# Kernel tuning notes

Measured on AMD Instinct MI355X. Metric: run time of the kernel, lower is better.

## Reference

```python
import jax, jax.numpy as jnp
import numpy as np

N_QUBITS = 8
DEPTH = 3
FEATURE_DIM = 512
NUM_CLASSES = 10
BATCH = 8192
CDTYPE = jnp.complex64


def _ry_batched(theta):
    # theta: (B,) -> (B,2,2) real RY matrices cast to complex
    c = jnp.cos(theta / 2)
    s = jnp.sin(theta / 2)
    row0 = jnp.stack([c, -s], axis=-1)
    row1 = jnp.stack([s, c], axis=-1)
    return jnp.stack([row0, row1], axis=-2).astype(CDTYPE)


def _ry(theta):
    c = jnp.cos(theta / 2).astype(CDTYPE)
    s = jnp.sin(theta / 2).astype(CDTYPE)
    return jnp.stack([jnp.stack([c, -s]), jnp.stack([s, c])])


def _rx(theta):
    c = jnp.cos(theta / 2).astype(CDTYPE)
    js = (-1j) * jnp.sin(theta / 2).astype(CDTYPE)
    return jnp.stack([jnp.stack([c, js]), jnp.stack([js, c])])


def _apply_1q(state, U, q, n):
    # state: (B, 2,...,2) little-endian: axis (n - q) holds qubit q's bit
    ax = n - q
    sm = jnp.moveaxis(state, ax, -1)
    if U.ndim == 3:  # per-batch gate
        new = jnp.einsum('b...k,bjk->b...j', sm, U)
    else:  # shared gate
        new = jnp.einsum('...k,jk->...j', sm, U)
    return jnp.moveaxis(new, -1, ax)


def _cnot(state, c, t, n):
    ax_c = n - c
    ax_t = n - t
    s0, s1 = jnp.split(state, 2, axis=ax_c)
    s1 = jnp.flip(s1, axis=ax_t)  # X on target where control=1
    return jnp.concatenate([s0, s1], axis=ax_c)


def _quantum_expect(angles, qnn_w, n=N_QUBITS, depth=DEPTH):
    # angles: (B, n) encoding angles; qnn_w: (depth*n*3,) circuit weights
    B = angles.shape[0]
    state = jnp.zeros((B,) + (2,) * n, CDTYPE)
    state = state.at[(slice(None),) + (0,) * n].set(1.0)
    # RY encoding layer (batched angles)
    for q in range(n):
        state = _apply_1q(state, _ry_batched(angles[:, q]), q, n)
    wr = qnn_w.reshape(depth, n, 3)
    for l in range(depth):
        for q in range(n):
            state = _apply_1q(state, _rx(wr[l, q, 0]), q, n)
            state = _apply_1q(state, _ry(wr[l, q, 1]), q, n)
            state = _apply_1q(state, _rx(wr[l, q, 2]), q, n)
        for q in range(n - 1):
            state = _cnot(state, q, q + 1, n)
        state = _cnot(state, n - 1, 0, n)
    # PauliZ expectation per qubit: sum probs weighted by (+1, -1) on that qubit's axis
    p = state.real ** 2 + state.imag ** 2  # (B, 2,...,2) real
    z = jnp.array([1.0, -1.0], p.dtype)
    outs = []
    for q in range(n):
        ax = n - q
        sign = z.reshape((1,) * ax + (2,) + (1,) * q)
        outs.append(jnp.sum(p * sign, axis=tuple(range(1, n + 1))))
    return jnp.stack(outs, axis=-1)  # (B, n)


def setup_inputs() -> dict:
    key = jax.random.key(0)
    k1, k2, k3, k4, k5 = jax.random.split(key, 5)
    x = jax.random.normal(k1, (BATCH, FEATURE_DIM), jnp.float32)
    bound_p = 1.0 / np.sqrt(FEATURE_DIM)
    proj_w = jax.random.uniform(k2, (N_QUBITS, FEATURE_DIM), jnp.float32, -bound_p, bound_p)
    qnn_w = 0.01 * jax.random.normal(k3, (DEPTH * N_QUBITS * 3,), jnp.float32)
    bound_o = 1.0 / np.sqrt(N_QUBITS)
    out_w = jax.random.uniform(k4, (NUM_CLASSES, N_QUBITS), jnp.float32, -bound_o, bound_o)
    out_b = jax.random.uniform(k5, (NUM_CLASSES,), jnp.float32, -bound_o, bound_o)
    return {'x': x, 'proj_w': proj_w, 'qnn_w': qnn_w, 'out_w': out_w, 'out_b': out_b}


def reference(x, proj_w, qnn_w, out_w, out_b):
    angles = jnp.tanh(x @ proj_w.T) * (jnp.pi / 2)  # (B, n_qubits)
    q_out = _quantum_expect(angles, qnn_w)          # (B, n_qubits)
    return q_out @ out_w.T + out_b                  # (B, num_classes)
```

## Files before the change

### kernel.cpp

```cpp
#include <hip/hip_runtime.h>
#include <math.h>

#define NQ 8
#define NDEPTH 3
#define FEAT 512
#define NCLS 10
#define NBATCH 8192


template <int CTRL, int ROW_MASK>
__device__ __forceinline__ float dpp_term(float v) {
    return __int_as_float(__builtin_amdgcn_update_dpp(
        0, __float_as_int(v), CTRL, ROW_MASK, 0xf, true));
}

__device__ __forceinline__ float wave_sum_bcast(float v) {
    v += dpp_term<0x111, 0xf>(v);
    v += dpp_term<0x112, 0xf>(v);
    v += dpp_term<0x114, 0xf>(v);
    v += dpp_term<0x118, 0xf>(v);
    v += dpp_term<0x142, 0xa>(v);
    v += dpp_term<0x143, 0xc>(v);
    return __int_as_float(__builtin_amdgcn_readlane(__float_as_int(v), 63));
}

__device__ __forceinline__ float bcastlane(float v, int srclane) {
    return __int_as_float(__builtin_amdgcn_readlane(__float_as_int(v), srclane));
}

template <int CTRL>
__device__ __forceinline__ float dpp_xor(float v) {
    return __int_as_float(__builtin_amdgcn_update_dpp(
        0, __float_as_int(v), CTRL, 0xf, 0xf, true));
}

__device__ __forceinline__ float fast_tanh(float v) {
    float e = __expf(2.f * v);
    return 1.f - 2.f / (e + 1.f);
}

__device__ __forceinline__ void cgate_pair(const float* __restrict__ u,
        float& r0, float& i0, float& r1, float& i1) {
    float nr0 = u[0]*r0 - u[1]*i0 + u[2]*r1 - u[3]*i1;
    float ni0 = u[0]*i0 + u[1]*r0 + u[2]*i1 + u[3]*r1;
    float nr1 = u[4]*r0 - u[5]*i0 + u[6]*r1 - u[7]*i1;
    float ni1 = u[4]*i0 + u[5]*r0 + u[6]*i1 + u[7]*r1;
    r0 = nr0; i0 = ni0; r1 = nr1; i1 = ni1;
}

__device__ __forceinline__ void cgate_shfl(const float* __restrict__ u, int bit,
        int mask, float (&re)[4], float (&im)[4]) {
    float dr  = bit ? u[6] : u[0], di = bit ? u[7] : u[1];
    float orr = bit ? u[4] : u[2], oi = bit ? u[5] : u[3];
#pragma unroll
    for (int j = 0; j < 4; j++) {
        float pr = __shfl_xor(re[j], mask);
        float pi = __shfl_xor(im[j], mask);
        float nr = dr*re[j] - di*im[j] + orr*pr - oi*pi;
        float ni = dr*im[j] + di*re[j] + orr*pi + oi*pr;
        re[j] = nr; im[j] = ni;
    }
}

template <int CTRL>
__device__ __forceinline__ void cgate_dpp(const float* __restrict__ u, int bit,
        float (&re)[4], float (&im)[4]) {
    float dr  = bit ? u[6] : u[0], di = bit ? u[7] : u[1];
    float orr = bit ? u[4] : u[2], oi = bit ? u[5] : u[3];
#pragma unroll
    for (int j = 0; j < 4; j++) {
        float pr = dpp_xor<CTRL>(re[j]);
        float pi = dpp_xor<CTRL>(im[j]);
        float nr = dr*re[j] - di*im[j] + orr*pr - oi*pi;
        float ni = dr*im[j] + di*re[j] + orr*pi + oi*pr;
        re[j] = nr; im[j] = ni;
    }
}

__global__ __launch_bounds__(256) void qsim_kernel(
        const float* __restrict__ x, const float* __restrict__ proj_w,
        const float* __restrict__ qnn_w, const float* __restrict__ out_w,
        const float* __restrict__ out_b, float* __restrict__ out) {
    __shared__ float gl[NDEPTH * NQ * 8];

    int tid = threadIdx.x;
    if (tid < NDEPTH * NQ) {
        float t0 = 0.5f * qnn_w[tid * 3 + 0];
        float t1 = 0.5f * qnn_w[tid * 3 + 1];
        float t2 = 0.5f * qnn_w[tid * 3 + 2];
        float c0 = cosf(t0), s0 = sinf(t0);
        float c1 = cosf(t1), s1 = sinf(t1);
        float c2 = cosf(t2), s2 = sinf(t2);
        float m00r =  c1 * c0, m00i =  s1 * s0;
        float m01r = -s1 * c0, m01i = -c1 * s0;
        float m10r =  s1 * c0, m10i = -c1 * s0;
        float m11r =  c1 * c0, m11i = -s1 * s0;
        float* g = gl + tid * 8;
        g[0] =  c2 * m00r + s2 * m10i;  g[1] =  c2 * m00i - s2 * m10r;
        g[2] =  c2 * m01r + s2 * m11i;  g[3] =  c2 * m01i - s2 * m11r;
        g[4] =  s2 * m00i + c2 * m10r;  g[5] = -s2 * m00r + c2 * m10i;
        g[6] =  s2 * m01i + c2 * m11r;  g[7] = -s2 * m01r + c2 * m11i;
    }
    __syncthreads();

    int lane = tid & 63;
    int b = blockIdx.x * 4 + (tid >> 6);

    const float4* xr4 = (const float4*)(x + (size_t)b * FEAT);
    float4 xa = xr4[lane], xb = xr4[lane + 64];
    float dq[8];
#pragma unroll
    for (int q = 0; q < 8; q++) {
        const float4* pw4 = (const float4*)(proj_w + q * FEAT);
        float4 wa = pw4[lane], wb = pw4[lane + 64];
        float acc = xa.x*wa.x + xa.y*wa.y + xa.z*wa.z + xa.w*wa.w
                  + xb.x*wb.x + xb.y*wb.y + xb.z*wb.z + xb.w*wb.w;
        dq[q] = wave_sum_bcast(acc);
    }
    int qsel = lane >> 3;
    float a0 = (qsel & 4) ? dq[4] : dq[0];
    float a1 = (qsel & 4) ? dq[5] : dq[1];
    float a2 = (qsel & 4) ? dq[6] : dq[2];
    float a3 = (qsel & 4) ? dq[7] : dq[3];
    float b0 = (qsel & 2) ? a2 : a0;
    float b1 = (qsel & 2) ? a3 : a1;
    float dsel = (qsel & 1) ? b1 : b0;
    float th = fast_tanh(dsel) * 0.78539816339744830962f;
    float se = __sinf(th), ce = __cosf(th);
    float cq[8], sq[8];
#pragma unroll
    for (int q = 0; q < 8; q++) {
        cq[q] = bcastlane(ce, q * 8);
        sq[q] = bcastlane(se, q * 8);
    }

    float F = 1.f;
#pragma unroll
    for (int q = 2; q < 8; q++) {
        int bit = (lane >> (q - 2)) & 1;
        F *= bit ? sq[q] : cq[q];
    }
    float re[4], im[4];
    re[0] = F * cq[0] * cq[1];
    re[1] = F * sq[0] * cq[1];
    re[2] = F * cq[0] * sq[1];
    re[3] = F * sq[0] * sq[1];
    im[0] = im[1] = im[2] = im[3] = 0.f;

#pragma unroll
    for (int l = 0; l < NDEPTH; l++) {
        const float* g = gl + l * NQ * 8;
        cgate_pair(g, re[0], im[0], re[1], im[1]);
        cgate_pair(g, re[2], im[2], re[3], im[3]);
        cgate_pair(g + 8,  re[0], im[0], re[2], im[2]);
        cgate_pair(g + 8,  re[1], im[1], re[3], im[3]);
        cgate_dpp<0xB1>(g + 16, lane & 1,        re, im);
        cgate_dpp<0x4E>(g + 24, (lane >> 1) & 1, re, im);
        cgate_shfl(g + 32, (lane >> 2) & 1, 4,  re, im);
        cgate_shfl(g + 40, (lane >> 3) & 1, 8,  re, im);
        cgate_shfl(g + 48, (lane >> 4) & 1, 16, re, im);
        cgate_shfl(g + 56, (lane >> 5) & 1, 32, re, im);
        { float t = re[1]; re[1] = re[3]; re[3] = t;
          t = im[1]; im[1] = im[3]; im[3] = t; }
        int base  = lane ^ ((lane << 1) & 63);
        int base2 = base ^ 1;
        re[0] = __shfl(re[0], base);  im[0] = __shfl(im[0], base);
        re[1] = __shfl(re[1], base);  im[1] = __shfl(im[1], base);
        re[2] = __shfl(re[2], base2); im[2] = __shfl(im[2], base2);
        re[3] = __shfl(re[3], base2); im[3] = __shfl(im[3], base2);
        int bit5 = (lane >> 5) & 1;
        {
            float t0 = bit5 ? re[1] : re[0], t1 = bit5 ? re[0] : re[1];
            float t2 = bit5 ? re[3] : re[2], t3 = bit5 ? re[2] : re[3];
            re[0] = t0; re[1] = t1; re[2] = t2; re[3] = t3;
            t0 = bit5 ? im[1] : im[0]; t1 = bit5 ? im[0] : im[1];
            t2 = bit5 ? im[3] : im[2]; t3 = bit5 ? im[2] : im[3];
            im[0] = t0; im[1] = t1; im[2] = t2; im[3] = t3;
        }
    }

    float p0 = re[0]*re[0] + im[0]*im[0];
    float p1 = re[1]*re[1] + im[1]*im[1];
    float p2 = re[2]*re[2] + im[2]*im[2];
    float p3 = re[3]*re[3] + im[3]*im[3];
    float pt = p0 + p1 + p2 + p3;
    float eq[8];
    eq[0] = wave_sum_bcast(p0 - p1 + p2 - p3);
    eq[1] = wave_sum_bcast(p0 + p1 - p2 - p3);
#pragma unroll
    for (int q = 2; q < 8; q++) {
        int bit = (lane >> (q - 2)) & 1;
        eq[q] = wave_sum_bcast(bit ? -pt : pt);
    }

    if (lane < NCLS) {
        const float* wrow = out_w + lane * NQ;
        float acc = out_b[lane];
#pragma unroll
        for (int q = 0; q < 8; q++) acc = fmaf(eq[q], wrow[q], acc);
        out[(size_t)b * NCLS + lane] = acc;
    }
}

extern "C" void kernel_launch(void* const* d_in, const int* in_sizes, int n_in,
                              void* d_out, int out_size, void* d_ws, size_t ws_size,
                              hipStream_t stream) {
    const float* x      = (const float*)d_in[0];
    const float* proj_w = (const float*)d_in[1];
    const float* qnn_w  = (const float*)d_in[2];
    const float* out_w  = (const float*)d_in[3];
    const float* out_b  = (const float*)d_in[4];
    float* out = (float*)d_out;

    qsim_kernel<<<NBATCH / 4, 256, 0, stream>>>(x, proj_w, qnn_w, out_w, out_b, out);
}
```

Baseline: 83.88 us.

## Process two samples per wave with swizzle-based gates and segmented reductions

Each wavefront now simulates two batch samples, interleaving their gate updates so cross-lane latency is hidden and proj_w loads are shared. Eight separate wave reductions for the projection are replaced by a segmented transpose-reduce, and the readout uses a butterfly with sign multipliers instead of six full reductions. Shuffles with masks 4/8/16 become ds_swizzle ops, gate matrices are loaded as float4 from LDS, and cos/sin use fast intrinsics. The cost is higher register pressure and half the grid size, with fewer waves available to hide latency.

```diff
diff --git a/kernel.cpp b/kernel.cpp
--- a/kernel.cpp
+++ b/kernel.cpp
@@ -34,12 +34,24 @@
         0, __float_as_int(v), CTRL, 0xf, 0xf, true));
 }
 
+template <int PAT>
+__device__ __forceinline__ float swz(float v) {
+    return __int_as_float(__builtin_amdgcn_ds_swizzle(__float_as_int(v), PAT));
+}
+
 __device__ __forceinline__ float fast_tanh(float v) {
     float e = __expf(2.f * v);
     return 1.f - 2.f / (e + 1.f);
 }
 
-__device__ __forceinline__ void cgate_pair(const float* __restrict__ u,
+__device__ __forceinline__ void load_u(const float* g, float (&u)[8]) {
+    float4 a = *(const float4*)g;
+    float4 b = *(const float4*)(g + 4);
+    u[0] = a.x; u[1] = a.y; u[2] = a.z; u[3] = a.w;
+    u[4] = b.x; u[5] = b.y; u[6] = b.z; u[7] = b.w;
+}
+
+__device__ __forceinline__ void cgate_pair(const float (&u)[8],
         float& r0, float& i0, float& r1, float& i1) {
     float nr0 = u[0]*r0 - u[1]*i0 + u[2]*r1 - u[3]*i1;
     float ni0 = u[0]*i0 + u[1]*r0 + u[2]*i1 + u[3]*r1;
@@ -48,22 +60,37 @@
     r0 = nr0; i0 = ni0; r1 = nr1; i1 = ni1;
 }
 
-__device__ __forceinline__ void cgate_shfl(const float* __restrict__ u, int bit,
-        int mask, float (&re)[4], float (&im)[4]) {
+template <int PAT>
+__device__ __forceinline__ void cgate_swz(const float (&u)[8], int bit,
+        float (&re)[4], float (&im)[4]) {
     float dr  = bit ? u[6] : u[0], di = bit ? u[7] : u[1];
     float orr = bit ? u[4] : u[2], oi = bit ? u[5] : u[3];
 #pragma unroll
     for (int j = 0; j < 4; j++) {
-        float pr = __shfl_xor(re[j], mask);
-        float pi = __shfl_xor(im[j], mask);
+        float pr = swz<PAT>(re[j]);
+        float pi = swz<PAT>(im[j]);
         float nr = dr*re[j] - di*im[j] + orr*pr - oi*pi;
         float ni = dr*im[j] + di*re[j] + orr*pi + oi*pr;
         re[j] = nr; im[j] = ni;
     }
 }
 
+__device__ __forceinline__ void cgate_shfl32(const float (&u)[8], int bit,
+        float (&re)[4], float (&im)[4]) {
+    float dr  = bit ? u[6] : u[0], di = bit ? u[7] : u[1];
+    float orr = bit ? u[4] : u[2], oi = bit ? u[5] : u[3];
+#pragma unroll
+    for (int j = 0; j < 4; j++) {
+        float pr = __shfl_xor(re[j], 32);
+        float pi = __shfl_xor(im[j], 32);
+        float nr = dr*re[j] - di*im[j] + orr*pr - oi*pi;
+        float ni = dr*im[j] + di*re[j] + orr*pi + oi*pr;
+        re[j] = nr; im[j] = ni;
+    }
+}
+
 template <int CTRL>
-__device__ __forceinline__ void cgate_dpp(const float* __restrict__ u, int bit,
+__device__ __forceinline__ void cgate_dpp(const float (&u)[8], int bit,
         float (&re)[4], float (&im)[4]) {
     float dr  = bit ? u[6] : u[0], di = bit ? u[7] : u[1];
     float orr = bit ? u[4] : u[2], oi = bit ? u[5] : u[3];
@@ -77,7 +104,77 @@
     }
 }
 
-__global__ __launch_bounds__(256) void qsim_kernel(
+__device__ __forceinline__ float seg_reduce8(const float (&a)[8], int lane) {
+    bool h5 = (lane & 32) != 0, h4 = (lane & 16) != 0, h3 = (lane & 8) != 0;
+    float r4[4];
+#pragma unroll
+    for (int k = 0; k < 4; k++) {
+        float snd = h5 ? a[k] : a[4 + k];
+        float rcv = __shfl_xor(snd, 32);
+        float kp  = h5 ? a[4 + k] : a[k];
+        r4[k] = kp + rcv;
+    }
+    float r2[2];
+#pragma unroll
+    for (int k = 0; k < 2; k++) {
+        float snd = h4 ? r4[k] : r4[2 + k];
+        float rcv = swz<0x401F>(snd);
+        float kp  = h4 ? r4[2 + k] : r4[k];
+        r2[k] = kp + rcv;
+    }
+    float snd = h3 ? r2[0] : r2[1];
+    float rcv = swz<0x201F>(snd);
+    float kp  = h3 ? r2[1] : r2[0];
+    float r = kp + rcv;
+    r += swz<0x101F>(r);
+    r += dpp_xor<0x4E>(r);
+    r += dpp_xor<0xB1>(r);
+    return r;
+}
+
+__device__ __forceinline__ void cnot_ladder(int lane, int base, int base2,
+        float (&re)[4], float (&im)[4]) {
+    float t = re[1]; re[1] = re[3]; re[3] = t;
+    t = im[1]; im[1] = im[3]; im[3] = t;
+    re[0] = __shfl(re[0], base);  im[0] = __shfl(im[0], base);
+    re[1] = __shfl(re[1], base);  im[1] = __shfl(im[1], base);
+    re[2] = __shfl(re[2], base2); im[2] = __shfl(im[2], base2);
+    re[3] = __shfl(re[3], base2); im[3] = __shfl(im[3], base2);
+    int bit5 = (lane >> 5) & 1;
+    float t0 = bit5 ? re[1] : re[0], t1 = bit5 ? re[0] : re[1];
+    float t2 = bit5 ? re[3] : re[2], t3 = bit5 ? re[2] : re[3];
+    re[0] = t0; re[1] = t1; re[2] = t2; re[3] = t3;
+    t0 = bit5 ? im[1] : im[0]; t1 = bit5 ? im[0] : im[1];
+    t2 = bit5 ? im[3] : im[2]; t3 = bit5 ? im[2] : im[3];
+    im[0] = t0; im[1] = t1; im[2] = t2; im[3] = t3;
+}
+
+__device__ __forceinline__ void readout(const float (&re)[4], const float (&im)[4],
+        float sg1, float sg2, float sg4, float sg8, float sg16, float sg32,
+        float (&eq)[8]) {
+    float p0 = re[0]*re[0] + im[0]*im[0];
+    float p1 = re[1]*re[1] + im[1]*im[1];
+    float p2 = re[2]*re[2] + im[2]*im[2];
+    float p3 = re[3]*re[3] + im[3]*im[3];
+    float pt = p0 + p1 + p2 + p3;
+    eq[0] = wave_sum_bcast(p0 - p1 + p2 - p3);
+    eq[1] = wave_sum_bcast(p0 + p1 - p2 - p3);
+    float w = pt;
+    w = fmaf(sg1,  w, dpp_xor<0xB1>(w));
+    w = fmaf(sg2,  w, dpp_xor<0x4E>(w));
+    w = fmaf(sg4,  w, swz<0x101F>(w));
+    w = fmaf(sg8,  w, swz<0x201F>(w));
+    w = fmaf(sg16, w, swz<0x401F>(w));
+    w = fmaf(sg32, w, __shfl_xor(w, 32));
+    eq[2] = bcastlane(w, 1);
+    eq[3] = bcastlane(w, 2);
+    eq[4] = bcastlane(w, 4);
+    eq[5] = bcastlane(w, 8);
+    eq[6] = bcastlane(w, 16);
+    eq[7] = bcastlane(w, 32);
+}
+
+__global__ __launch_bounds__(256, 4) void qsim_kernel(
         const float* __restrict__ x, const float* __restrict__ proj_w,
         const float* __restrict__ qnn_w, const float* __restrict__ out_w,
         const float* __restrict__ out_b, float* __restrict__ out) {
@@ -88,9 +185,9 @@
         float t0 = 0.5f * qnn_w[tid * 3 + 0];
         float t1 = 0.5f * qnn_w[tid * 3 + 1];
         float t2 = 0.5f * qnn_w[tid * 3 + 2];
-        float c0 = cosf(t0), s0 = sinf(t0);
-        float c1 = cosf(t1), s1 = sinf(t1);
-        float c2 = cosf(t2), s2 = sinf(t2);
+        float c0 = __cosf(t0), s0 = __sinf(t0);
+        float c1 = __cosf(t1), s1 = __sinf(t1);
+        float c2 = __cosf(t2), s2 = __sinf(t2);
         float m00r =  c1 * c0, m00i =  s1 * s0;
         float m01r = -s1 * c0, m01i = -c1 * s0;
         float m10r =  s1 * c0, m10i = -c1 * s0;
@@ -104,101 +201,119 @@
     __syncthreads();
 
     int lane = tid & 63;
-    int b = blockIdx.x * 4 + (tid >> 6);
-
-    const float4* xr4 = (const float4*)(x + (size_t)b * FEAT);
-    float4 xa = xr4[lane], xb = xr4[lane + 64];
-    float dq[8];
+    int wid  = tid >> 6;
+    int b0 = blockIdx.x * 8 + wid * 2;
+    int b1 = b0 + 1;
+
+    const float4* xA = (const float4*)(x + (size_t)b0 * FEAT);
+    const float4* xB = (const float4*)(x + (size_t)b1 * FEAT);
+    float4 xa0 = xA[lane], xb0 = xA[lane + 64];
+    float4 xa1 = xB[lane], xb1 = xB[lane + 64];
+    float acc0[8], acc1[8];
 #pragma unroll
     for (int q = 0; q < 8; q++) {
         const float4* pw4 = (const float4*)(proj_w + q * FEAT);
         float4 wa = pw4[lane], wb = pw4[lane + 64];
-        float acc = xa.x*wa.x + xa.y*wa.y + xa.z*wa.z + xa.w*wa.w
-                  + xb.x*wb.x + xb.y*wb.y + xb.z*wb.z + xb.w*wb.w;
-        dq[q] = wave_sum_bcast(acc);
-    }
-    int qsel = lane >> 3;
-    float a0 = (qsel & 4) ? dq[4] : dq[0];
-    float a1 = (qsel & 4) ? dq[5] : dq[1];
-    float a2 = (qsel & 4) ? dq[6] : dq[2];
-    float a3 = (qsel & 4) ? dq[7] : dq[3];
-    float b0 = (qsel & 2) ? a2 : a0;
-    float b1 = (qsel & 2) ? a3 : a1;
-    float dsel = (qsel & 1) ? b1 : b0;
-    float th = fast_tanh(dsel) * 0.78539816339744830962f;
-    float se = __sinf(th), ce = __cosf(th);
-    float cq[8], sq[8];
+        acc0[q] = xa0.x*wa.x + xa0.y*wa.y + xa0.z*wa.z + xa0.w*wa.w
+                + xb0.x*wb.x + xb0.y*wb.y + xb0.z*wb.z + xb0.w*wb.w;
+        acc1[q] = xa1.x*wa.x + xa1.y*wa.y + xa1.z*wa.z + xa1.w*wa.w
+                + xb1.x*wb.x + xb1.y*wb.y + xb1.z*wb.z + xb1.w*wb.w;
+    }
+    float d0 = seg_reduce8(acc0, lane);
+    float d1 = seg_reduce8(acc1, lane);
+    float th0 = fast_tanh(d0) * 0.78539816339744830962f;
+    float th1 = fast_tanh(d1) * 0.78539816339744830962f;
+    float se0 = __sinf(th0), ce0 = __cosf(th0);
+    float se1 = __sinf(th1), ce1 = __cosf(th1);
+    float cq0[8], sq0[8], cq1[8], sq1[8];
 #pragma unroll
     for (int q = 0; q < 8; q++) {
-        cq[q] = bcastlane(ce, q * 8);
-        sq[q] = bcastlane(se, q * 8);
-    }
-
-    float F = 1.f;
+        cq0[q] = bcastlane(ce0, q * 8);
+        sq0[q] = bcastlane(se0, q * 8);
+        cq1[q] = bcastlane(ce1, q * 8);
+        sq1[q] = bcastlane(se1, q * 8);
+    }
+
+    float F0 = 1.f, F1 = 1.f;
 #pragma unroll
     for (int q = 2; q < 8; q++) {
         int bit = (lane >> (q - 2)) & 1;
-        F *= bit ? sq[q] : cq[q];
-    }
-    float re[4], im[4];
-    re[0] = F * cq[0] * cq[1];
-    re[1] = F * sq[0] * cq[1];
-    re[2] = F * cq[0] * sq[1];
-    re[3] = F * sq[0] * sq[1];
-    im[0] = im[1] = im[2] = im[3] = 0.f;
-
+        F0 *= bit ? sq0[q] : cq0[q];
+        F1 *= bit ? sq1[q] : cq1[q];
+    }
+    float re0[4], im0[4], re1[4], im1[4];
+    re0[0] = F0 * cq0[0] * cq0[1];
+    re0[1] = F0 * sq0[0] * cq0[1];
+    re0[2] = F0 * cq0[0] * sq0[1];
+    re0[3] = F0 * sq0[0] * sq0[1];
+    re1[0] = F1 * cq1[0] * cq1[1];
+    re1[1] = F1 * sq1[0] * cq1[1];
+    re1[2] = F1 * cq1[0] * sq1[1];
+    re1[3] = F1 * sq1[0] * sq1[1];
+    im0[0] = im0[1] = im0[2] = im0[3] = 0.f;
+    im1[0] = im1[1] = im1[2] = im1[3] = 0.f;
+
+    int base  = lane ^ ((lane << 1) & 63);
+    int base2 = base ^ 1;
 #pragma unroll
     for (int l = 0; l < NDEPTH; l++) {
-        const float* g = gl + l * NQ * 8;
-        cgate_pair(g, re[0], im[0], re[1], im[1]);
-        cgate_pair(g, re[2], im[2], re[3], im[3]);
-        cgate_pair(g + 8,  re[0], im[0], re[2], im[2]);
-        cgate_pair(g + 8,  re[1], im[1], re[3], im[3]);
-        cgate_dpp<0xB1>(g + 16, lane & 1,        re, im);
-        cgate_dpp<0x4E>(g + 24, (lane >> 1) & 1, re, im);
-        cgate_shfl(g + 32, (lane >> 2) & 1, 4,  re, im);
-        cgate_shfl(g + 40, (lane >> 3) & 1, 8,  re, im);
-        cgate_shfl(g + 48, (lane >> 4) & 1, 16, re, im);
-        cgate_shfl(g + 56, (lane >> 5) & 1, 32, re, im);
-        { float t = re[1]; re[1] = re[3]; re[3] = t;
-          t = im[1]; im[1] = im[3]; im[3] = t; }
-        int base  = lane ^ ((lane << 1) & 63);
-        int base2 = base ^ 1;
-        re[0] = __shfl(re[0], base);  im[0] = __shfl(im[0], base);
-        re[1] = __shfl(re[1], base);  im[1] = __shfl(im[1], base);
-        re[2] = __shfl(re[2], base2); im[2] = __shfl(im[2], base2);
-        re[3] = __shfl(re[3], base2); im[3] = __shfl(im[3], base2);
-        int bit5 = (lane >> 5) & 1;
-        {
-            float t0 = bit5 ? re[1] : re[0], t1 = bit5 ? re[0] : re[1];
-            float t2 = bit5 ? re[3] : re[2], t3 = bit5 ? re[2] : re[3];
-            re[0] = t0; re[1] = t1; re[2] = t2; re[3] = t3;
-            t0 = bit5 ? im[1] : im[0]; t1 = bit5 ? im[0] : im[1];
-            t2 = bit5 ? im[3] : im[2]; t3 = bit5 ? im[2] : im[3];
-            im[0] = t0; im[1] = t1; im[2] = t2; im[3] = t3;
-        }
-    }
-
-    float p0 = re[0]*re[0] + im[0]*im[0];
-    float p1 = re[1]*re[1] + im[1]*im[1];
-    float p2 = re[2]*re[2] + im[2]*im[2];
-    float p3 = re[3]*re[3] + im[3]*im[3];
-    float pt = p0 + p1 + p2 + p3;
-    float eq[8];
-    eq[0] = wave_sum_bcast(p0 - p1 + p2 - p3);
-    eq[1] = wave_sum_bcast(p0 + p1 - p2 - p3);
-#pragma unroll
-    for (int q = 2; q < 8; q++) {
-        int bit = (lane >> (q - 2)) & 1;
-        eq[q] = wave_sum_bcast(bit ? -pt : pt);
-    }
+        const float* gb = gl + l * NQ * 8;
+        float u[8];
+        load_u(gb + 0, u);
+        cgate_pair(u, re0[0], im0[0], re0[1], im0[1]);
+        cgate_pair(u, re0[2], im0[2], re0[3], im0[3]);
+        cgate_pair(u, re1[0], im1[0], re1[1], im1[1]);
+        cgate_pair(u, re1[2], im1[2], re1[3], im1[3]);
+        load_u(gb + 8, u);
+        cgate_pair(u, re0[0], im0[0], re0[2], im0[2]);
+        cgate_pair(u, re0[1], im0[1], re0[3], im0[3]);
+        cgate_pair(u, re1[0], im1[0], re1[2], im1[2]);
+        cgate_pair(u, re1[1], im1[1], re1[3], im1[3]);
+        load_u(gb + 16, u);
+        cgate_dpp<0xB1>(u, lane & 1, re0, im0);
+        cgate_dpp<0xB1>(u, lane & 1, re1, im1);
+        load_u(gb + 24, u);
+        cgate_dpp<0x4E>(u, (lane >> 1) & 1, re0, im0);
+        cgate_dpp<0x4E>(u, (lane >> 1) & 1, re1, im1);
+        load_u(gb + 32, u);
+        cgate_swz<0x101F>(u, (lane >> 2) & 1, re0, im0);
+        cgate_swz<0x101F>(u, (lane >> 2) & 1, re1, im1);
+        load_u(gb + 40, u);
+        cgate_swz<0x201F>(u, (lane >> 3) & 1, re0, im0);
+        cgate_swz<0x201F>(u, (lane >> 3) & 1, re1, im1);
+        load_u(gb + 48, u);
+        cgate_swz<0x401F>(u, (lane >> 4) & 1, re0, im0);
+        cgate_swz<0x401F>(u, (lane >> 4) & 1, re1, im1);
+        load_u(gb + 56, u);
+        cgate_shfl32(u, (lane >> 5) & 1, re0, im0);
+        cgate_shfl32(u, (lane >> 5) & 1, re1, im1);
+        cnot_ladder(lane, base, base2, re0, im0);
+        cnot_ladder(lane, base, base2, re1, im1);
+    }
+
+    float sg1  = (lane & 1)  ? -1.f : 1.f;
+    float sg2  = (lane & 2)  ? -1.f : 1.f;
+    float sg4  = (lane & 4)  ? -1.f : 1.f;
+    float sg8  = (lane & 8)  ? -1.f : 1.f;
+    float sg16 = (lane & 16) ? -1.f : 1.f;
+    float sg32 = (lane & 32) ? -1.f : 1.f;
+    float eA[8], eB[8];
+    readout(re0, im0, sg1, sg2, sg4, sg8, sg16, sg32, eA);
+    readout(re1, im1, sg1, sg2, sg4, sg8, sg16, sg32, eB);
 
     if (lane < NCLS) {
         const float* wrow = out_w + lane * NQ;
         float acc = out_b[lane];
 #pragma unroll
-        for (int q = 0; q < 8; q++) acc = fmaf(eq[q], wrow[q], acc);
-        out[(size_t)b * NCLS + lane] = acc;
+        for (int q = 0; q < 8; q++) acc = fmaf(eA[q], wrow[q], acc);
+        out[(size_t)b0 * NCLS + lane] = acc;
+    } else if (lane >= 32 && lane < 32 + NCLS) {
+        int c = lane - 32;
+        const float* wrow = out_w + c * NQ;
+        float acc = out_b[c];
+#pragma unroll
+        for (int q = 0; q < 8; q++) acc = fmaf(eB[q], wrow[q], acc);
+        out[(size_t)b1 * NCLS + c] = acc;
     }
 }
 
@@ -212,5 +327,5 @@
     const float* out_b  = (const float*)d_in[4];
     float* out = (float*)d_out;
 
-    qsim_kernel<<<NBATCH / 4, 256, 0, stream>>>(x, proj_w, qnn_w, out_w, out_b, out);
-}
+    qsim_kernel<<<NBATCH / 8, 256, 0, stream>>>(x, proj_w, qnn_w, out_w, out_b, out);
+}
```

New measurement: 84.05 us. About the same (+0.2%).
